# Kernel optimization log

Measured on AMD Instinct MI355X. Metric: run time of the kernel, lower is better.

## Reference

```python
import jax, jax.numpy as jnp
import numpy as np

NUM_HEADS = 12


def get_rel_pos(q_size, k_size, rel_pos):
    # rel_pos: (2*max(q,k)-1, C). Here q_size==k_size so no interpolation needed.
    q_coords = jnp.arange(q_size)[:, None] * max(k_size / q_size, 1.0)
    k_coords = jnp.arange(k_size)[None, :] * max(q_size / k_size, 1.0)
    rel = (q_coords - k_coords) + (k_size - 1) * max(q_size / k_size, 1.0)
    return rel_pos[rel.astype(jnp.int32)]  # (q_size, k_size, C)


def add_decomposed_rel_pos(attn, q, rel_pos_h, rel_pos_w, q_size, k_size):
    q_h, q_w = q_size
    k_h, k_w = k_size
    Rh = get_rel_pos(q_h, k_h, rel_pos_h)  # (q_h,k_h,C)
    Rw = get_rel_pos(q_w, k_w, rel_pos_w)  # (q_w,k_w,C)
    B, _, C = q.shape  # B = num_heads * batch
    r_q = q.reshape(B, q_h, q_w, C)
    rel_h = jnp.einsum('bhwc,hkc->bhwk', r_q, Rh)  # (B,q_h,q_w,k_h)
    rel_w = jnp.einsum('bhwc,wkc->bhwk', r_q, Rw)  # (B,q_h,q_w,k_w)
    attn = attn.reshape(B, q_h, q_w, k_h, k_w)
    attn = attn + rel_h[:, :, :, :, None] + rel_w[:, :, :, None, :]
    return attn.reshape(B, q_h * q_w, k_h * k_w)


def setup_inputs() -> dict:
    key = jax.random.key(0)
    ks = jax.random.split(key, 7)
    B, H, W, dim = 128, 14, 14, 768
    head_dim = dim // NUM_HEADS
    return {
        'x': jax.random.normal(ks[0], (B, H, W, dim), dtype=jnp.float32),
        'qkv_w': jax.random.normal(ks[1], (dim, 3 * dim), dtype=jnp.float32) * 0.02,
        'qkv_b': jax.random.normal(ks[2], (3 * dim,), dtype=jnp.float32) * 0.02,
        'proj_w': jax.random.normal(ks[3], (dim, dim), dtype=jnp.float32) * 0.02,
        'proj_b': jax.random.normal(ks[4], (dim,), dtype=jnp.float32) * 0.02,
        'rel_pos_h': jax.random.normal(ks[5], (2 * H - 1, head_dim), dtype=jnp.float32) * 0.02,
        'rel_pos_w': jax.random.normal(ks[6], (2 * W - 1, head_dim), dtype=jnp.float32) * 0.02,
    }


def reference(x, qkv_w, qkv_b, proj_w, proj_b, rel_pos_h, rel_pos_w):
    B, H, W, dim = x.shape
    nh = NUM_HEADS
    hd = dim // nh
    scale = hd ** -0.5
    L = H * W
    # qkv projection: (B,H,W,3*dim) -> (3, nh*B, L, hd)
    qkv = x.reshape(B, L, dim) @ qkv_w + qkv_b
    qkv = qkv.reshape(B, L, 3, nh, hd)
    qkv = jnp.transpose(qkv, (2, 3, 0, 1, 4)).reshape(3, nh * B, L, hd)
    q, k, v = qkv[0], qkv[1], qkv[2]
    attn = jnp.einsum('bqc,bkc->bqk', q * scale, k)  # (nh*B, L, L)
    attn = add_decomposed_rel_pos(attn, q, rel_pos_h, rel_pos_w, (H, W), (H, W))
    attn = jax.nn.softmax(attn, axis=-1)
    out = jnp.einsum('bqk,bkc->bqc', attn, v)  # (nh*B, L, hd)
    out = out.reshape(nh, B, H, W, hd)
    out = jnp.transpose(out, (1, 2, 3, 0, 4)).reshape(B, H, W, dim)
    return out @ proj_w + proj_b
```

## Files before the change

kernel.cpp:

```cpp
#include <hip/hip_runtime.h>
#include <stdint.h>

typedef unsigned short u16;
typedef __bf16 bf16x8 __attribute__((ext_vector_type(8)));
typedef u16 u16x8 __attribute__((ext_vector_type(8)));
typedef float f32x4 __attribute__((ext_vector_type(4)));

#define MFMA16(a,b,c) __builtin_amdgcn_mfma_f32_16x16x32_bf16((a),(b),(c),0,0,0)
#define GLOAD16(gp, lp) __builtin_amdgcn_global_load_lds( \
    (const __attribute__((address_space(1))) void*)(gp), \
    (__attribute__((address_space(3))) void*)(lp), 16, 0, 0)

__device__ __forceinline__ u16 f2bf(float f) {
  union { float f; uint32_t u; } v; v.f = f;
  return (u16)((v.u + 0x7FFFu + ((v.u >> 16) & 1u)) >> 16);
}
__device__ __forceinline__ float bits2f(uint32_t u) {
  union { uint32_t u; float f; } v; v.u = u; return v.f;
}
__device__ __forceinline__ uint32_t cvtpk(float lo, float hi) {
  uint32_t r;
  asm("v_cvt_pk_bf16_f32 %0, %1, %2" : "=v"(r) : "v"(lo), "v"(hi));
  return r;
}
__device__ __forceinline__ int4 pack8(const u16* v) {
  int4 r;
  r.x = (int)((uint32_t)v[0] | ((uint32_t)v[1] << 16));
  r.y = (int)((uint32_t)v[2] | ((uint32_t)v[3] << 16));
  r.z = (int)((uint32_t)v[4] | ((uint32_t)v[5] << 16));
  r.w = (int)((uint32_t)v[6] | ((uint32_t)v[7] << 16));
  return r;
}

__global__ void k_cvt(const float* __restrict__ in, u16* __restrict__ out, int n4) {
  int i = blockIdx.x * 256 + threadIdx.x;
  int stride = gridDim.x * 256;
  for (; i < n4; i += stride) {
    float4 v = reinterpret_cast<const float4*>(in)[i];
    ushort4 o;
    o.x = f2bf(v.x); o.y = f2bf(v.y); o.z = f2bf(v.z); o.w = f2bf(v.w);
    reinterpret_cast<ushort4*>(out)[i] = o;
  }
}

__global__ void k_transpose(const float* __restrict__ in, u16* __restrict__ out, int R, int C) {
  __shared__ float t[32][33];
  int tx = threadIdx.x & 31, ty = threadIdx.x >> 5;
  int c0 = blockIdx.x * 32, r0 = blockIdx.y * 32;
  #pragma unroll
  for (int i = 0; i < 4; i++)
    t[ty + i*8][tx] = in[(size_t)(r0 + ty + i*8) * C + (c0 + tx)];
  __syncthreads();
  #pragma unroll
  for (int i = 0; i < 4; i++)
    out[(size_t)(c0 + ty + i*8) * R + (r0 + tx)] = f2bf(t[tx][ty + i*8]);
}

template<int KDIM>
__device__ __forceinline__ void gemm_core(
    const u16* __restrict__ A, const u16* __restrict__ BT,
    int mt, int nt, f32x4 acc[4][4], u16* As, u16* Bs)
{
  int tid = threadIdx.x, lane = tid & 63, w = tid >> 6;
  int g = lane >> 4, c4 = lane & 15;
  int wr = w >> 1, wc = w & 1;
  int srow = lane >> 2;
  int pslot = (lane & 3) ^ ((lane >> 3) & 3);
  int rsel = g ^ ((c4 >> 1) & 3);
  const size_t abase = (size_t)(mt * 128) * KDIM;
  const size_t bbase = (size_t)(nt * 128) * KDIM;
  for (int kt = 0; kt < KDIM / 32; kt++) {
    __syncthreads();
    #pragma unroll
    for (int cc = 0; cc < 2; cc++) {
      int cid = w * 2 + cc;
      int row = cid * 16 + srow;
      GLOAD16(A + abase + (size_t)row * KDIM + kt * 32 + pslot * 8, As + cid * 512);
      GLOAD16(BT + bbase + (size_t)row * KDIM + kt * 32 + pslot * 8, Bs + cid * 512);
    }
    __syncthreads();
    bf16x8 af[4], bfv[4];
    #pragma unroll
    for (int f = 0; f < 4; f++) {
      af[f]  = *(const bf16x8*)(As + (wr * 64 + f * 16 + c4) * 32 + rsel * 8);
      bfv[f] = *(const bf16x8*)(Bs + (wc * 64 + f * 16 + c4) * 32 + rsel * 8);
    }
    #pragma unroll
    for (int fr = 0; fr < 4; fr++)
      #pragma unroll
      for (int fc = 0; fc < 4; fc++)
        acc[fr][fc] = MFMA16(af[fr], bfv[fc], acc[fr][fc]);
  }
}

__global__ __launch_bounds__(256, 3) void k_qkv_gemm(
    const u16* __restrict__ A, const u16* __restrict__ BT, const float* __restrict__ bias,
    u16* __restrict__ qo, u16* __restrict__ ko, u16* __restrict__ vo)
{
  __shared__ u16 As[128 * 32], Bs[128 * 32];
  int bid0 = blockIdx.x;
  int bid = (bid0 & 7) * 441 + (bid0 >> 3);
  int nt = bid % 18, mt = bid / 18;
  f32x4 z = {0.f, 0.f, 0.f, 0.f};
  f32x4 acc[4][4];
  #pragma unroll
  for (int i = 0; i < 4; i++)
    #pragma unroll
    for (int j = 0; j < 4; j++) acc[i][j] = z;
  gemm_core<768>(A, BT, mt, nt, acc, As, Bs);

  int tid = threadIdx.x, lane = tid & 63, w = tid >> 6;
  int g = lane >> 4, c4 = lane & 15;
  int wr = w >> 1, wc = w & 1;

  u16* dstA[4]; int ccA[4]; float bsA[4]; int hbA[4];
  #pragma unroll
  for (int fc = 0; fc < 4; fc++) {
    int n0 = nt * 128 + wc * 64 + fc * 16;
    int i3 = n0 / 768;
    int r = n0 - i3 * 768;
    dstA[fc] = (i3 == 0) ? qo : (i3 == 1) ? ko : vo;
    hbA[fc] = (r >> 6) * 128;
    ccA[fc] = (r & 63) + c4;
    bsA[fc] = bias[n0 + c4];
  }
  #pragma unroll
  for (int fr = 0; fr < 4; fr++) {
    #pragma unroll
    for (int j = 0; j < 4; j++) {
      int m = mt * 128 + wr * 64 + fr * 16 + g * 4 + j;
      int bb = m / 196;
      int ll = m - bb * 196;
      #pragma unroll
      for (int fc = 0; fc < 4; fc++) {
        dstA[fc][(size_t)((hbA[fc] + bb) * 196 + ll) * 64 + ccA[fc]] =
            f2bf(acc[fr][fc][j] + bsA[fc]);
      }
    }
  }
}

__global__ __launch_bounds__(256, 3) void k_proj_gemm(
    const u16* __restrict__ A, const u16* __restrict__ BT, const float* __restrict__ bias,
    float* __restrict__ out)
{
  __shared__ u16 As[128 * 32], Bs[128 * 32];
  int bid0 = blockIdx.x;
  int bid = (bid0 & 7) * 147 + (bid0 >> 3);
  int nt = bid % 6, mt = bid / 6;
  f32x4 z = {0.f, 0.f, 0.f, 0.f};
  f32x4 acc[4][4];
  #pragma unroll
  for (int i = 0; i < 4; i++)
    #pragma unroll
    for (int j = 0; j < 4; j++) acc[i][j] = z;
  gemm_core<768>(A, BT, mt, nt, acc, As, Bs);

  int tid = threadIdx.x, lane = tid & 63, w = tid >> 6;
  int g = lane >> 4, c4 = lane & 15;
  int wr = w >> 1, wc = w & 1;
  #pragma unroll
  for (int fc = 0; fc < 4; fc++) {
    int n0 = nt * 128 + wc * 64 + fc * 16 + c4;
    float bs = bias[n0];
    #pragma unroll
    for (int fr = 0; fr < 4; fr++)
      #pragma unroll
      for (int j = 0; j < 4; j++) {
        int m = mt * 128 + wr * 64 + fr * 16 + g * 4 + j;
        out[(size_t)m * 768 + n0] = acc[fr][fc][j] + bs;
      }
  }
}

__global__ __launch_bounds__(256, 2) void k_attn(
    const u16* __restrict__ Q, const u16* __restrict__ Kg, const u16* __restrict__ Vg,
    const u16* __restrict__ RPH, const u16* __restrict__ RPW, u16* __restrict__ Ows)
{
  __shared__ u16 K64[208 * 64];
  __shared__ u16 Krel[208 * 40];
  __shared__ u16 VT[64 * 232];
  __shared__ u16 Qrel[4][16 * 40];

  int bh = blockIdx.x;
  int hh = bh >> 7, bb = bh & 127;
  int tid = threadIdx.x, lane = tid & 63, w = tid >> 6;
  int g = lane >> 4, c4 = lane & 15;

  const u16* kbase = Kg + (size_t)bh * 12544;
  const u16* vbase = Vg + (size_t)bh * 12544;
  const u16* qbase = Q + (size_t)bh * 12544;

  for (int ch = tid; ch < 1664; ch += 256) {
    int row = ch >> 3, s = ch & 7;
    u16 outv[8];
    if (row < 196) {
      u16x8 v = *(const u16x8*)(kbase + row * 64 + s * 8);
      #pragma unroll
      for (int e = 0; e < 8; e++)
        outv[e] = f2bf(bits2f((uint32_t)v[e] << 16) * 0.125f);
    } else {
      #pragma unroll
      for (int e = 0; e < 8; e++) outv[e] = 0;
    }
    *(int4*)(K64 + row * 64 + ((s ^ (row & 7)) * 8)) = pack8(outv);
  }

  if (tid < 208) {
    int k = tid;
    int kh = k / 14, kw2 = k - kh * 14;
    #pragma unroll
    for (int s = 0; s < 5; s++) {
      u16 vals[8];
      #pragma unroll
      for (int e = 0; e < 8; e++) {
        int c = s * 8 + e;
        u16 x = 0;
        if (k < 196) {
          if (c == kh) x = 0x3F80;
          else if (c == 14 + kw2) x = 0x3F80;
        } else {
          if (c == 28) x = 0x3F80;
        }
        vals[e] = x;
      }
      *(int4*)(Krel + k * 40 + s * 8) = pack8(vals);
    }
  }

  for (int i = tid; i < 2048; i += 256) {
    int chn = i >> 5, c = 192 + (i & 31);
    if (c >= 196) VT[chn * 232 + c] = 0;
  }
  for (int ch2 = tid; ch2 < 784; ch2 += 256) {
    int kp = ch2 >> 3, cb = ch2 & 7;
    int key = kp * 2, cz = cb * 8;
    u16x8 a = *(const u16x8*)(vbase + key * 64 + cz);
    u16x8 b2 = *(const u16x8*)(vbase + (key + 1) * 64 + cz);
    int kk = key & 31;
    int colp = (key >> 5) * 32 + ((kk & 15) >> 2) * 8 + (kk & 3) + ((kk >> 4) << 2);
    #pragma unroll
    for (int j = 0; j < 8; j++) {
      uint32_t pk = (uint32_t)a[j] | ((uint32_t)b2[j] << 16);
      *(uint32_t*)(VT + (cz + j) * 232 + colp) = pk;
    }
  }
  __syncthreads();

  int t1 = 16 + c4; if (t1 > 26) t1 = 26;
  bf16x8 rh00 = *(const bf16x8*)(RPH + c4 * 64 + g * 8);
  bf16x8 rh01 = *(const bf16x8*)(RPH + c4 * 64 + 32 + g * 8);
  bf16x8 rh10 = *(const bf16x8*)(RPH + t1 * 64 + g * 8);
  bf16x8 rh11 = *(const bf16x8*)(RPH + t1 * 64 + 32 + g * 8);
  bf16x8 rw00 = *(const bf16x8*)(RPW + c4 * 64 + g * 8);
  bf16x8 rw01 = *(const bf16x8*)(RPW + c4 * 64 + 32 + g * 8);
  bf16x8 rw10 = *(const bf16x8*)(RPW + t1 * 64 + g * 8);
  bf16x8 rw11 = *(const bf16x8*)(RPW + t1 * 64 + 32 + g * 8);

  f32x4 z4 = {0.f, 0.f, 0.f, 0.f};

  for (int qt = w; qt < 13; qt += 4) {
    int qi = qt * 16 + c4;
    int qrow = qi > 195 ? 195 : qi;
    bf16x8 qa0 = *(const bf16x8*)(qbase + qrow * 64 + g * 8);
    bf16x8 qa1 = *(const bf16x8*)(qbase + qrow * 64 + 32 + g * 8);

    u16* Qr = (u16*)Qrel[w];
    {
      int4 zz = {0, 0, 0, 0};
      *(int4*)(Qr + lane * 8) = zz;
      if (lane < 16) *(int4*)(Qr + 512 + lane * 8) = zz;
      if (g == 0) Qr[c4 * 40 + 28] = f2bf(-30000.f);
    }

    int qh = qi / 14;
    int qwv = qi - qh * 14;

    f32x4 e0 = MFMA16(rh00, qa0, z4); e0 = MFMA16(rh01, qa1, e0);
    f32x4 e1 = MFMA16(rh10, qa0, z4); e1 = MFMA16(rh11, qa1, e1);
    #pragma unroll
    for (int tt = 0; tt < 2; tt++) {
      f32x4 e = tt ? e1 : e0;
      #pragma unroll
      for (int j = 0; j < 4; j++) {
        int t = tt * 16 + 4 * g + j;
        int kh = qh + 13 - t;
        if ((unsigned)kh <= 13u) Qr[c4 * 40 + kh] = f2bf(e[j]);
      }
    }
    f32x4 f0 = MFMA16(rw00, qa0, z4); f0 = MFMA16(rw01, qa1, f0);
    f32x4 f1 = MFMA16(rw10, qa0, z4); f1 = MFMA16(rw11, qa1, f1);
    #pragma unroll
    for (int tt = 0; tt < 2; tt++) {
      f32x4 e = tt ? f1 : f0;
      #pragma unroll
      for (int j = 0; j < 4; j++) {
        int t = tt * 16 + 4 * g + j;
        int kw3 = qwv + 13 - t;
        if ((unsigned)kw3 <= 13u) Qr[c4 * 40 + 14 + kw3] = f2bf(e[j]);
      }
    }

    bf16x8 qrelB = *(const bf16x8*)(Qr + c4 * 40 + g * 8);

    f32x4 St[13];
    #pragma unroll
    for (int i = 0; i < 13; i++) {
      int key = i * 16 + c4;
      const u16* kr = K64 + key * 64;
      int sw = key & 7;
      bf16x8 kb0 = *(const bf16x8*)(kr + ((g ^ sw) * 8));
      bf16x8 kb1 = *(const bf16x8*)(kr + (((4 + g) ^ sw) * 8));
      f32x4 acc = MFMA16(kb0, qa0, z4);
      acc = MFMA16(kb1, qa1, acc);
      bf16x8 krl = *(const bf16x8*)(Krel + key * 40 + g * 8);
      St[i] = MFMA16(krl, qrelB, acc);
    }

    float mx = -3.0e38f;
    #pragma unroll
    for (int i = 0; i < 13; i++)
      #pragma unroll
      for (int j = 0; j < 4; j++) mx = fmaxf(mx, St[i][j]);
    mx = fmaxf(mx, __shfl_xor(mx, 16));
    mx = fmaxf(mx, __shfl_xor(mx, 32));

    float ls = 0.f;
    f32x4 O[4] = {z4, z4, z4, z4};
    #pragma unroll
    for (int p = 0; p < 7; p++) {
      float pe[8];
      #pragma unroll
      for (int j2 = 0; j2 < 4; j2++) { pe[j2] = __expf(St[2 * p][j2] - mx); ls += pe[j2]; }
      if (p < 6) {
        #pragma unroll
        for (int j2 = 0; j2 < 4; j2++) { pe[4 + j2] = __expf(St[2 * p + 1][j2] - mx); ls += pe[4 + j2]; }
      } else {
        #pragma unroll
        for (int j2 = 0; j2 < 4; j2++) pe[4 + j2] = 0.f;
      }
      union { uint32_t u[4]; bf16x8 v; } pb;
      pb.u[0] = cvtpk(pe[0], pe[1]);
      pb.u[1] = cvtpk(pe[2], pe[3]);
      pb.u[2] = cvtpk(pe[4], pe[5]);
      pb.u[3] = cvtpk(pe[6], pe[7]);
      #pragma unroll
      for (int ct = 0; ct < 4; ct++) {
        bf16x8 va = *(const bf16x8*)(VT + (ct * 16 + c4) * 232 + p * 32 + g * 8);
        O[ct] = MFMA16(va, pb.v, O[ct]);
      }
    }
    ls += __shfl_xor(ls, 16);
    ls += __shfl_xor(ls, 32);

    if (qi < 196) {
      float inv = 1.f / ls;
      size_t obase = (size_t)(bb * 196 + qi) * 768 + hh * 64;
      #pragma unroll
      for (int ct = 0; ct < 4; ct++) {
        uint32_t o0 = cvtpk(O[ct][0] * inv, O[ct][1] * inv);
        uint32_t o1 = cvtpk(O[ct][2] * inv, O[ct][3] * inv);
        uint2 ov = {o0, o1};
        *(uint2*)(Ows + obase + ct * 16 + g * 4) = ov;
      }
    }
  }
}

extern "C" void kernel_launch(void* const* d_in, const int* in_sizes, int n_in,
                              void* d_out, int out_size, void* d_ws, size_t ws_size,
                              hipStream_t stream) {
  (void)in_sizes; (void)n_in; (void)out_size; (void)ws_size;
  const float* x      = (const float*)d_in[0];
  const float* qkv_w  = (const float*)d_in[1];
  const float* qkv_b  = (const float*)d_in[2];
  const float* proj_w = (const float*)d_in[3];
  const float* proj_b = (const float*)d_in[4];
  const float* rph    = (const float*)d_in[5];
  const float* rpw    = (const float*)d_in[6];
  float* out = (float*)d_out;
  char* ws = (char*)d_ws;

  u16* xb   = (u16*)(ws);
  u16* wT   = (u16*)(ws + 38535168);
  u16* pT   = (u16*)(ws + 42074112);
  u16* rphb = (u16*)(ws + 43253760);
  u16* rpwb = (u16*)(ws + 43257856);
  u16* qws  = (u16*)(ws + 43261952);
  u16* kws  = (u16*)(ws + 81797120);
  u16* vws  = (u16*)(ws + 120332288);
  u16* Ows  = xb;

  k_cvt<<<2048, 256, 0, stream>>>(x, xb, 4816896);
  k_cvt<<<2, 256, 0, stream>>>(rph, rphb, 432);
  k_cvt<<<2, 256, 0, stream>>>(rpw, rpwb, 432);
  k_transpose<<<dim3(72, 24), 256, 0, stream>>>(qkv_w, wT, 768, 2304);
  k_transpose<<<dim3(24, 24), 256, 0, stream>>>(proj_w, pT, 768, 768);
  k_qkv_gemm<<<196 * 18, 256, 0, stream>>>(xb, wT, qkv_b, qws, kws, vws);
  k_attn<<<1536, 256, 0, stream>>>(qws, kws, vws, rphb, rpwb, Ows);
  k_proj_gemm<<<196 * 6, 256, 0, stream>>>(Ows, pT, proj_b, out);
}
```

Measured before the change: 275.3 us.

## Replace QKV GEMM with 256x256 multi-stage pipelined kernel and stage attention output via LDS

Swaps the 128x128 QKV GEMM for a 512-thread 256x256 tile kernel. It uses a 4-slot LDS ring buffer with direct global-to-LDS loads issued three k-steps ahead, split A/B prefetch, and an XCD-aware block remap. The epilogue writes each head's output through LDS so global stores become 16-byte coalesced rows. The attention kernel likewise stages its output tile through a swizzled per-wave LDS buffer for coalesced stores, and shrinks the V transpose padding. The cost is 128KB of LDS per block, which limits occupancy, and fewer, larger blocks, which risks tail imbalance.

```diff
diff --git a/kernel.cpp b/kernel.cpp
--- a/kernel.cpp
+++ b/kernel.cpp
@@ -54,6 +54,126 @@
   #pragma unroll
   for (int i = 0; i < 4; i++)
     out[(size_t)(c0 + ty + i*8) * R + (r0 + tx)] = f2bf(t[tx][ty + i*8]);
+}
+
+__global__ __launch_bounds__(512, 2) void k_qkv256(
+    const u16* __restrict__ A, const u16* __restrict__ BT, const float* __restrict__ bias,
+    u16* __restrict__ qo, u16* __restrict__ ko, u16* __restrict__ vo)
+{
+  __shared__ u16 SMEM[65536];
+
+  int bid0 = blockIdx.x;
+  int xcd = bid0 & 7, idx = bid0 >> 3;
+  int base = (xcd < 2) ? xcd * 111 : 2 * 111 + (xcd - 2) * 110;
+  int wgid = base + idx;
+  int mt = wgid / 9, nt = wgid - (wgid / 9) * 9;
+
+  int tid = threadIdx.x, lane = tid & 63, w = tid >> 6;
+  int g = lane >> 4, c4 = lane & 15;
+  int wr = w >> 2, wc = w & 3;
+
+  int c1 = tid, c2 = tid + 512;
+  int pr1 = c1 >> 3, sl1 = (c1 & 7) ^ (pr1 & 7);
+  int g1 = sl1 >> 1, row1 = pr1 * 2 + (sl1 & 1);
+  int pr2 = c2 >> 3, sl2 = (c2 & 7) ^ (pr2 & 7);
+  int g2 = sl2 >> 1, row2 = pr2 * 2 + (sl2 & 1);
+
+  const u16* pA1 = A + (size_t)(mt * 256 + row1) * 768 + g1 * 8;
+  const u16* pA2 = A + (size_t)(mt * 256 + row2) * 768 + g2 * 8;
+  const u16* pB1 = BT + (size_t)(nt * 256 + row1) * 768 + g1 * 8;
+  const u16* pB2 = BT + (size_t)(nt * 256 + row2) * 768 + g2 * 8;
+
+  int prc = c4 >> 1;
+  int slotRd = (2 * g + (c4 & 1)) ^ prc;
+  int aoff = wr * 4096 + prc * 64 + slotRd * 8;
+  int boff = wc * 2048 + prc * 64 + slotRd * 8;
+
+  f32x4 acc[8][4];
+  f32x4 z4 = {0.f, 0.f, 0.f, 0.f};
+  #pragma unroll
+  for (int f = 0; f < 8; f++)
+    #pragma unroll
+    for (int fc = 0; fc < 4; fc++) acc[f][fc] = z4;
+
+  #pragma unroll
+  for (int kk = 0; kk < 3; kk++) {
+    u16* dA = SMEM + (kk << 13);
+    GLOAD16(pA1 + kk * 32, dA + c1 * 8);
+    GLOAD16(pA2 + kk * 32, dA + c2 * 8);
+    u16* dB = SMEM + 32768 + (kk << 13);
+    GLOAD16(pB1 + kk * 32, dB + c1 * 8);
+    GLOAD16(pB2 + kk * 32, dB + c2 * 8);
+  }
+  asm volatile("s_waitcnt vmcnt(8)" ::: "memory");
+  __builtin_amdgcn_s_barrier();
+
+  for (int k = 0; k < 24; ++k) {
+    const u16* As = SMEM + ((k & 3) << 13);
+    const u16* Bs = SMEM + 32768 + ((k & 3) << 13);
+    bf16x8 bfr[4], afr[4];
+    #pragma unroll
+    for (int fc = 0; fc < 4; fc++) bfr[fc] = *(const bf16x8*)(Bs + boff + fc * 512);
+    #pragma unroll
+    for (int f = 0; f < 4; f++) afr[f] = *(const bf16x8*)(As + aoff + f * 512);
+    if (k < 21) {
+      u16* d = SMEM + (((k + 3) & 3) << 13);
+      GLOAD16(pA1 + (k + 3) * 32, d + c1 * 8);
+      GLOAD16(pA2 + (k + 3) * 32, d + c2 * 8);
+      asm volatile("s_waitcnt vmcnt(6)" ::: "memory");
+    } else if (k == 21) {
+      asm volatile("s_waitcnt vmcnt(0)" ::: "memory");
+    }
+    __builtin_amdgcn_s_barrier();
+    #pragma unroll
+    for (int f = 0; f < 4; f++)
+      #pragma unroll
+      for (int fc = 0; fc < 4; fc++)
+        acc[f][fc] = MFMA16(afr[f], bfr[fc], acc[f][fc]);
+
+    #pragma unroll
+    for (int f = 0; f < 4; f++) afr[f] = *(const bf16x8*)(As + aoff + (4 + f) * 512);
+    if (k < 21) {
+      u16* d = SMEM + 32768 + (((k + 3) & 3) << 13);
+      GLOAD16(pB1 + (k + 3) * 32, d + c1 * 8);
+      GLOAD16(pB2 + (k + 3) * 32, d + c2 * 8);
+      asm volatile("s_waitcnt vmcnt(6)" ::: "memory");
+    }
+    __builtin_amdgcn_s_barrier();
+    #pragma unroll
+    for (int f = 0; f < 4; f++)
+      #pragma unroll
+      for (int fc = 0; fc < 4; fc++)
+        acc[4 + f][fc] = MFMA16(afr[f], bfr[fc], acc[4 + f][fc]);
+  }
+
+  __builtin_amdgcn_s_barrier();
+  u16* Ob = SMEM + w * 8192;
+
+  int i3 = nt / 3;
+  u16* dst = (i3 == 0) ? qo : (i3 == 1) ? ko : vo;
+  int head = (nt - i3 * 3) * 4 + wc;
+  float bsv[4];
+  #pragma unroll
+  for (int fc = 0; fc < 4; fc++) bsv[fc] = bias[nt * 256 + wc * 64 + fc * 16 + c4];
+
+  #pragma unroll
+  for (int f = 0; f < 8; f++)
+    #pragma unroll
+    for (int fc = 0; fc < 4; fc++)
+      #pragma unroll
+      for (int j = 0; j < 4; j++)
+        Ob[(f * 16 + 4 * g + j) * 64 + fc * 16 + c4] = f2bf(acc[f][fc][j] + bsv[fc]);
+
+  int m0 = mt * 256 + wr * 128;
+  #pragma unroll
+  for (int it2 = 0; it2 < 16; ++it2) {
+    int cc = it2 * 64 + lane;
+    int row = cc >> 3, kc = cc & 7;
+    int mm = m0 + row;
+    int bb2 = mm / 196, ll = mm - bb2 * 196;
+    int4 v = *(const int4*)(Ob + row * 64 + kc * 8);
+    *(int4*)(dst + ((size_t)((head * 128 + bb2) * 196 + ll)) * 64 + kc * 8) = v;
+  }
 }
 
 template<int KDIM>
@@ -93,53 +213,6 @@
   }
 }
 
-__global__ __launch_bounds__(256, 3) void k_qkv_gemm(
-    const u16* __restrict__ A, const u16* __restrict__ BT, const float* __restrict__ bias,
-    u16* __restrict__ qo, u16* __restrict__ ko, u16* __restrict__ vo)
-{
-  __shared__ u16 As[128 * 32], Bs[128 * 32];
-  int bid0 = blockIdx.x;
-  int bid = (bid0 & 7) * 441 + (bid0 >> 3);
-  int nt = bid % 18, mt = bid / 18;
-  f32x4 z = {0.f, 0.f, 0.f, 0.f};
-  f32x4 acc[4][4];
-  #pragma unroll
-  for (int i = 0; i < 4; i++)
-    #pragma unroll
-    for (int j = 0; j < 4; j++) acc[i][j] = z;
-  gemm_core<768>(A, BT, mt, nt, acc, As, Bs);
-
-  int tid = threadIdx.x, lane = tid & 63, w = tid >> 6;
-  int g = lane >> 4, c4 = lane & 15;
-  int wr = w >> 1, wc = w & 1;
-
-  u16* dstA[4]; int ccA[4]; float bsA[4]; int hbA[4];
-  #pragma unroll
-  for (int fc = 0; fc < 4; fc++) {
-    int n0 = nt * 128 + wc * 64 + fc * 16;
-    int i3 = n0 / 768;
-    int r = n0 - i3 * 768;
-    dstA[fc] = (i3 == 0) ? qo : (i3 == 1) ? ko : vo;
-    hbA[fc] = (r >> 6) * 128;
-    ccA[fc] = (r & 63) + c4;
-    bsA[fc] = bias[n0 + c4];
-  }
-  #pragma unroll
-  for (int fr = 0; fr < 4; fr++) {
-    #pragma unroll
-    for (int j = 0; j < 4; j++) {
-      int m = mt * 128 + wr * 64 + fr * 16 + g * 4 + j;
-      int bb = m / 196;
-      int ll = m - bb * 196;
-      #pragma unroll
-      for (int fc = 0; fc < 4; fc++) {
-        dstA[fc][(size_t)((hbA[fc] + bb) * 196 + ll) * 64 + ccA[fc]] =
-            f2bf(acc[fr][fc][j] + bsA[fc]);
-      }
-    }
-  }
-}
-
 __global__ __launch_bounds__(256, 3) void k_proj_gemm(
     const u16* __restrict__ A, const u16* __restrict__ BT, const float* __restrict__ bias,
     float* __restrict__ out)
@@ -173,14 +246,15 @@
   }
 }
 
+#define VP 216
 __global__ __launch_bounds__(256, 2) void k_attn(
     const u16* __restrict__ Q, const u16* __restrict__ Kg, const u16* __restrict__ Vg,
     const u16* __restrict__ RPH, const u16* __restrict__ RPW, u16* __restrict__ Ows)
 {
   __shared__ u16 K64[208 * 64];
   __shared__ u16 Krel[208 * 40];
-  __shared__ u16 VT[64 * 232];
-  __shared__ u16 Qrel[4][16 * 40];
+  __shared__ u16 VT[64 * VP];
+  __shared__ u16 QO[4][1024];
 
   int bh = blockIdx.x;
   int hh = bh >> 7, bb = bh & 127;
@@ -205,7 +279,6 @@
     }
     *(int4*)(K64 + row * 64 + ((s ^ (row & 7)) * 8)) = pack8(outv);
   }
-
   if (tid < 208) {
     int k = tid;
     int kh = k / 14, kw2 = k - kh * 14;
@@ -227,10 +300,9 @@
       *(int4*)(Krel + k * 40 + s * 8) = pack8(vals);
     }
   }
-
-  for (int i = tid; i < 2048; i += 256) {
-    int chn = i >> 5, c = 192 + (i & 31);
-    if (c >= 196) VT[chn * 232 + c] = 0;
+  for (int i = tid; i < 64 * 20; i += 256) {
+    int chn = i / 20, col = 196 + (i - chn * 20);
+    VT[chn * VP + col] = 0;
   }
   for (int ch2 = tid; ch2 < 784; ch2 += 256) {
     int kp = ch2 >> 3, cb = ch2 & 7;
@@ -242,7 +314,7 @@
     #pragma unroll
     for (int j = 0; j < 8; j++) {
       uint32_t pk = (uint32_t)a[j] | ((uint32_t)b2[j] << 16);
-      *(uint32_t*)(VT + (cz + j) * 232 + colp) = pk;
+      *(uint32_t*)(VT + (cz + j) * VP + colp) = pk;
     }
   }
   __syncthreads();
@@ -258,6 +330,7 @@
   bf16x8 rw11 = *(const bf16x8*)(RPW + t1 * 64 + 32 + g * 8);
 
   f32x4 z4 = {0.f, 0.f, 0.f, 0.f};
+  int sw = c4 & 7;
 
   for (int qt = w; qt < 13; qt += 4) {
     int qi = qt * 16 + c4;
@@ -265,13 +338,13 @@
     bf16x8 qa0 = *(const bf16x8*)(qbase + qrow * 64 + g * 8);
     bf16x8 qa1 = *(const bf16x8*)(qbase + qrow * 64 + 32 + g * 8);
 
-    u16* Qr = (u16*)Qrel[w];
+    u16* Qr = (u16*)QO[w];
     {
       int4 zz = {0, 0, 0, 0};
-      *(int4*)(Qr + lane * 8) = zz;
-      if (lane < 16) *(int4*)(Qr + 512 + lane * 8) = zz;
-      if (g == 0) Qr[c4 * 40 + 28] = f2bf(-30000.f);
-    }
+      int zr = lane >> 2, zs = lane & 3;
+      *(int4*)(Qr + zr * 64 + ((zs ^ (zr & 7)) * 8)) = zz;
+    }
+    if (g == 0) Qr[c4 * 64 + (28 ^ (sw << 3))] = f2bf(-30000.f);
 
     int qh = qi / 14;
     int qwv = qi - qh * 14;
@@ -285,7 +358,7 @@
       for (int j = 0; j < 4; j++) {
         int t = tt * 16 + 4 * g + j;
         int kh = qh + 13 - t;
-        if ((unsigned)kh <= 13u) Qr[c4 * 40 + kh] = f2bf(e[j]);
+        if ((unsigned)kh <= 13u) Qr[c4 * 64 + (kh ^ (sw << 3))] = f2bf(e[j]);
       }
     }
     f32x4 f0 = MFMA16(rw00, qa0, z4); f0 = MFMA16(rw01, qa1, f0);
@@ -297,20 +370,20 @@
       for (int j = 0; j < 4; j++) {
         int t = tt * 16 + 4 * g + j;
         int kw3 = qwv + 13 - t;
-        if ((unsigned)kw3 <= 13u) Qr[c4 * 40 + 14 + kw3] = f2bf(e[j]);
-      }
-    }
-
-    bf16x8 qrelB = *(const bf16x8*)(Qr + c4 * 40 + g * 8);
+        if ((unsigned)kw3 <= 13u) Qr[c4 * 64 + ((14 + kw3) ^ (sw << 3))] = f2bf(e[j]);
+      }
+    }
+
+    bf16x8 qrelB = *(const bf16x8*)(Qr + c4 * 64 + ((g ^ sw) * 8));
 
     f32x4 St[13];
     #pragma unroll
     for (int i = 0; i < 13; i++) {
       int key = i * 16 + c4;
       const u16* kr = K64 + key * 64;
-      int sw = key & 7;
-      bf16x8 kb0 = *(const bf16x8*)(kr + ((g ^ sw) * 8));
-      bf16x8 kb1 = *(const bf16x8*)(kr + (((4 + g) ^ sw) * 8));
+      int swk = key & 7;
+      bf16x8 kb0 = *(const bf16x8*)(kr + ((g ^ swk) * 8));
+      bf16x8 kb1 = *(const bf16x8*)(kr + (((4 + g) ^ swk) * 8));
       f32x4 acc = MFMA16(kb0, qa0, z4);
       acc = MFMA16(kb1, qa1, acc);
       bf16x8 krl = *(const bf16x8*)(Krel + key * 40 + g * 8);
@@ -346,22 +419,29 @@
       pb.u[3] = cvtpk(pe[6], pe[7]);
       #pragma unroll
       for (int ct = 0; ct < 4; ct++) {
-        bf16x8 va = *(const bf16x8*)(VT + (ct * 16 + c4) * 232 + p * 32 + g * 8);
+        bf16x8 va = *(const bf16x8*)(VT + (ct * 16 + c4) * VP + p * 32 + g * 8);
         O[ct] = MFMA16(va, pb.v, O[ct]);
       }
     }
     ls += __shfl_xor(ls, 16);
     ls += __shfl_xor(ls, 32);
 
-    if (qi < 196) {
-      float inv = 1.f / ls;
-      size_t obase = (size_t)(bb * 196 + qi) * 768 + hh * 64;
-      #pragma unroll
-      for (int ct = 0; ct < 4; ct++) {
-        uint32_t o0 = cvtpk(O[ct][0] * inv, O[ct][1] * inv);
-        uint32_t o1 = cvtpk(O[ct][2] * inv, O[ct][3] * inv);
-        uint2 ov = {o0, o1};
-        *(uint2*)(Ows + obase + ct * 16 + g * 4) = ov;
+    float inv = 1.f / ls;
+    #pragma unroll
+    for (int ct = 0; ct < 4; ct++) {
+      uint32_t o0 = cvtpk(O[ct][0] * inv, O[ct][1] * inv);
+      uint32_t o1 = cvtpk(O[ct][2] * inv, O[ct][3] * inv);
+      uint2 ov = {o0, o1};
+      *(uint2*)(Qr + c4 * 64 + ((ct * 16 + g * 4) ^ (sw << 3))) = ov;
+    }
+    #pragma unroll
+    for (int it = 0; it < 2; ++it) {
+      int cc = it * 64 + lane;
+      int row = cc >> 3, kc = cc & 7;
+      int q = qt * 16 + row;
+      if (q < 196) {
+        int4 v = *(const int4*)(Qr + row * 64 + ((kc ^ (row & 7)) * 8));
+        *(int4*)(Ows + (size_t)(bb * 196 + q) * 768 + hh * 64 + kc * 8) = v;
       }
     }
   }
@@ -396,7 +476,7 @@
   k_cvt<<<2, 256, 0, stream>>>(rpw, rpwb, 432);
   k_transpose<<<dim3(72, 24), 256, 0, stream>>>(qkv_w, wT, 768, 2304);
   k_transpose<<<dim3(24, 24), 256, 0, stream>>>(proj_w, pT, 768, 768);
-  k_qkv_gemm<<<196 * 18, 256, 0, stream>>>(xb, wT, qkv_b, qws, kws, vws);
+  k_qkv256<<<882, 512, 0, stream>>>(xb, wT, qkv_b, qws, kws, vws);
   k_attn<<<1536, 256, 0, stream>>>(qws, kws, vws, rphb, rpwb, Ows);
   k_proj_gemm<<<196 * 6, 256, 0, stream>>>(Ows, pT, proj_b, out);
 }
```

Result: no change. 275.2 us (-0.0%).
